# Performance work log

Hardware: AMD Instinct MI355X
Metric: run time of the kernel (lower is better)

## Reference

```python
import jax, jax.numpy as jnp
import numpy as np
from itertools import permutations

B, T, A, NIN = 10, 100, 20, 4096
NIMG, NATT, NPHYS = 1024, 512, 256


def _build_perm():
    # all 190 unordered pairs of 20 agents, lexicographically sorted (matches np.unique on sorted perms)
    perm = np.unique(np.sort(np.array(list(permutations(range(A), 2))), axis=1), axis=0)  # (190, 2)
    # for each agent k: the 19 pair-indices containing k, ordered (k in col0 first, then col1) as in torch code
    perm_ind = np.stack([
        np.hstack((np.where(perm[:, 0] == k)[0], np.where(perm[:, 1] == k)[0])) for k in range(A)
    ])  # (20, 19)
    return perm.astype(np.int32), perm_ind.astype(np.int32)

PERM, PERM_IND = _build_perm()


def setup_inputs() -> dict:
    key = jax.random.key(0)
    ks = jax.random.split(key, 7)
    def lin(k, out_f, in_f):
        return (jax.random.normal(k, (out_f, in_f), jnp.float32) / np.float32(np.sqrt(in_f)))
    return {
        "x": jax.random.normal(ks[0], (B, T, A, NIN), jnp.float32),
        "world_coord_feat": jax.random.normal(ks[1], (B, T, A, 13), jnp.float32),
        "W_glob": lin(ks[2], NIMG, NIN), "b_glob": jnp.zeros((NIMG,), jnp.float32),
        "W_loc": lin(ks[3], NATT, NIN), "b_loc": jnp.zeros((NATT,), jnp.float32),
        "W_phys": lin(ks[4], NPHYS, 26), "b_phys": jnp.zeros((NPHYS,), jnp.float32),
        "W_phys3": lin(ks[5], NPHYS, NPHYS), "b_phys3": jnp.zeros((NPHYS,), jnp.float32),
    }


def reference(x, world_coord_feat, W_glob, b_glob, W_loc, b_loc, W_phys, b_phys, W_phys3, b_phys3):
    pa = jnp.asarray(PERM)        # (190, 2)
    pind = jnp.asarray(PERM_IND)  # (20, 19)
    # global / local embeddings
    glob_embed = x[:, :, 0, :] @ W_glob.T + b_glob          # (B, T, NIMG)
    loc_embed = x[:, :, 1:, :] @ W_loc.T + b_loc            # (B, T, 19, NATT)
    # pairwise physical features: concat coords of both agents of each pair
    perm_feat = jnp.concatenate(
        [world_coord_feat[:, :, pa[:, 0], :], world_coord_feat[:, :, pa[:, 1], :]], axis=-1
    )                                                        # (B, T, 190, 26)
    # dropout layers are identity at inference; mask is computed but unused in original
    h1 = jax.nn.relu(perm_feat @ W_phys.T + b_phys)          # (B, T, 190, NPHYS)
    phys = h1 @ W_phys3.T + b_phys3                          # (B, T, 190, NPHYS)
    # per-agent gather of its 19 pairs + max-pool over pairs (fused segment-max)
    agent_tensor = jnp.max(phys[:, :, pind, :], axis=3)      # (B, T, 20, NPHYS)
    return glob_embed, loc_embed, agent_tensor
```

## Files before the change

### kernel.cpp

```cpp
#include <hip/hip_runtime.h>
#include <stdint.h>

typedef __bf16 bf16x8 __attribute__((ext_vector_type(8)));
typedef float  f32x4  __attribute__((ext_vector_type(4)));

__device__ __forceinline__ bf16x8 cvt8(const float* __restrict__ p) {
    float4 lo = *(const float4*)p;
    float4 hi = *(const float4*)(p + 4);
    bf16x8 r;
    r[0] = (__bf16)lo.x; r[1] = (__bf16)lo.y; r[2] = (__bf16)lo.z; r[3] = (__bf16)lo.w;
    r[4] = (__bf16)hi.x; r[5] = (__bf16)hi.y; r[6] = (__bf16)hi.z; r[7] = (__bf16)hi.w;
    return r;
}

__device__ __forceinline__ bf16x8 pack8(float4 lo, float4 hi) {
    bf16x8 r;
    r[0] = (__bf16)lo.x; r[1] = (__bf16)lo.y; r[2] = (__bf16)lo.z; r[3] = (__bf16)lo.w;
    r[4] = (__bf16)hi.x; r[5] = (__bf16)hi.y; r[6] = (__bf16)hi.z; r[7] = (__bf16)hi.w;
    return r;
}

__device__ __forceinline__ int pidx(int i, int j) {
    return i * 19 - (i * (i - 1)) / 2 + (j - i - 1);
}

template <int MODE, bool A_BF16, bool OUT_BF16>
__global__ __launch_bounds__(256) void gemm_bias_kernel(
    const void* __restrict__ Xv,
    const float* __restrict__ W,
    const float* __restrict__ bias,
    void* __restrict__ Cv,
    int M, int N, int K)
{
    __shared__ __bf16 As[64][40];
    __shared__ __bf16 Bs[64][40];

    const int tid  = threadIdx.x;
    const int srow = tid >> 2;
    const int scol = (tid & 3) << 3;

    int gmrow = (int)blockIdx.y * 64 + srow;
    int rA = gmrow < M ? gmrow : M - 1;
    size_t aoff;
    if (MODE == 0)      aoff = (size_t)rA * 81920;
    else if (MODE == 1) aoff = ((size_t)(rA / 19) * 20 + (size_t)(rA % 19) + 1) * 4096;
    else                aoff = (size_t)rA * (size_t)K;
    const float*  aptrF = (const float*)Xv  + aoff + scol;
    const __bf16* aptrH = (const __bf16*)Xv + aoff + scol;
    const float*  bptr  = W + (size_t)((int)blockIdx.x * 64 + srow) * (size_t)K + scol;

    const int w    = tid >> 6;
    const int lane = tid & 63;
    const int wm   = (w >> 1) * 32;
    const int wn   = (w & 1) * 32;
    const int l    = lane & 15;
    const int qk   = lane >> 4;
    const int q8   = qk * 8;

    f32x4 acc00 = {}, acc01 = {}, acc10 = {}, acc11 = {};

    for (int k0 = 0; k0 < K; k0 += 32) {
        bf16x8 av, bv;
        if (A_BF16) av = *(const bf16x8*)(aptrH + k0);
        else        av = cvt8(aptrF + k0);
        bv = cvt8(bptr + k0);
        __syncthreads();
        *(bf16x8*)&As[srow][scol] = av;
        *(bf16x8*)&Bs[srow][scol] = bv;
        __syncthreads();
        bf16x8 a0 = *(const bf16x8*)&As[wm + l][q8];
        bf16x8 a1 = *(const bf16x8*)&As[wm + 16 + l][q8];
        bf16x8 b0 = *(const bf16x8*)&Bs[wn + l][q8];
        bf16x8 b1 = *(const bf16x8*)&Bs[wn + 16 + l][q8];
        acc00 = __builtin_amdgcn_mfma_f32_16x16x32_bf16(a0, b0, acc00, 0, 0, 0);
        acc01 = __builtin_amdgcn_mfma_f32_16x16x32_bf16(a0, b1, acc01, 0, 0, 0);
        acc10 = __builtin_amdgcn_mfma_f32_16x16x32_bf16(a1, b0, acc10, 0, 0, 0);
        acc11 = __builtin_amdgcn_mfma_f32_16x16x32_bf16(a1, b1, acc11, 0, 0, 0);
    }

    const int colBase = (int)blockIdx.x * 64;
    const int rowBase = (int)blockIdx.y * 64;
    const float bias0 = bias[colBase + wn + l];
    const float bias1 = bias[colBase + wn + 16 + l];
    #pragma unroll
    for (int i = 0; i < 2; ++i) {
        f32x4 aj0 = (i == 0) ? acc00 : acc10;
        f32x4 aj1 = (i == 0) ? acc01 : acc11;
        #pragma unroll
        for (int r = 0; r < 4; ++r) {
            int row = rowBase + wm + i * 16 + qk * 4 + r;
            if (row < M) {
                size_t base = (size_t)row * (size_t)N + colBase + wn;
                float v0 = aj0[r] + bias0;
                float v1 = aj1[r] + bias1;
                if (OUT_BF16) {
                    ((__bf16*)Cv)[base + l]      = (__bf16)v0;
                    ((__bf16*)Cv)[base + 16 + l] = (__bf16)v1;
                } else {
                    ((float*)Cv)[base + l]      = v0;
                    ((float*)Cv)[base + 16 + l] = v1;
                }
            }
        }
    }
}

__global__ __launch_bounds__(256) void gemm_loc_v2(
    const float* __restrict__ X,
    const float* __restrict__ W,
    const float* __restrict__ bias,
    float* __restrict__ C)
{
    constexpr int M = 19000, N = 512, K = 4096;
    __shared__ __bf16 As[2][128][40];
    __shared__ __bf16 Bs[2][128][40];

    const int gx = 4, nwg = 596;
    int lid = (int)blockIdx.y * gx + (int)blockIdx.x;
    {
        int q = nwg >> 3, r = nwg & 7;
        int xcd = lid & 7, idx = lid >> 3;
        lid = (xcd < r ? xcd * (q + 1) : r * (q + 1) + (xcd - r) * q) + idx;
    }
    const int tx = lid % gx;
    const int ty = lid / gx;

    const int tid  = threadIdx.x;
    const int srow = tid >> 2;
    const int scol = (tid & 3) << 3;

    int gr0 = ty * 128 + srow;      int rA0 = gr0 < M ? gr0 : M - 1;
    int gr1 = gr0 + 64;             int rA1 = gr1 < M ? gr1 : M - 1;
    const float* aptr0 = X + ((size_t)(rA0 / 19) * 20 + (size_t)(rA0 % 19) + 1) * 4096 + scol;
    const float* aptr1 = X + ((size_t)(rA1 / 19) * 20 + (size_t)(rA1 % 19) + 1) * 4096 + scol;
    const float* bptr0 = W + (size_t)(tx * 128 + srow) * (size_t)K + scol;
    const float* bptr1 = W + (size_t)(tx * 128 + 64 + srow) * (size_t)K + scol;

    const int w    = tid >> 6;
    const int lane = tid & 63;
    const int wm   = (w >> 1) * 64;
    const int wn   = (w & 1) * 64;
    const int l    = lane & 15;
    const int qk   = lane >> 4;
    const int q8   = qk << 3;

    f32x4 acc[4][4];
    #pragma unroll
    for (int m = 0; m < 4; ++m)
        #pragma unroll
        for (int n = 0; n < 4; ++n) { f32x4 z = {0.f, 0.f, 0.f, 0.f}; acc[m][n] = z; }

    float4 sa0l, sa0h, sa1l, sa1h, sb0l, sb0h, sb1l, sb1h;

    sa0l = *(const float4*)(aptr0);     sa0h = *(const float4*)(aptr0 + 4);
    sa1l = *(const float4*)(aptr1);     sa1h = *(const float4*)(aptr1 + 4);
    sb0l = *(const float4*)(bptr0);     sb0h = *(const float4*)(bptr0 + 4);
    sb1l = *(const float4*)(bptr1);     sb1h = *(const float4*)(bptr1 + 4);
    *(bf16x8*)&As[0][srow][scol]      = pack8(sa0l, sa0h);
    *(bf16x8*)&As[0][srow + 64][scol] = pack8(sa1l, sa1h);
    *(bf16x8*)&Bs[0][srow][scol]      = pack8(sb0l, sb0h);
    *(bf16x8*)&Bs[0][srow + 64][scol] = pack8(sb1l, sb1h);

    int cur = 0;
    for (int i = 0; i < K / 32; ++i) {
        __syncthreads();
        if (i + 1 < K / 32) {
            int k0 = (i + 1) << 5;
            sa0l = *(const float4*)(aptr0 + k0); sa0h = *(const float4*)(aptr0 + k0 + 4);
            sa1l = *(const float4*)(aptr1 + k0); sa1h = *(const float4*)(aptr1 + k0 + 4);
            sb0l = *(const float4*)(bptr0 + k0); sb0h = *(const float4*)(bptr0 + k0 + 4);
            sb1l = *(const float4*)(bptr1 + k0); sb1h = *(const float4*)(bptr1 + k0 + 4);
        }
        bf16x8 af[4], bfr[4];
        #pragma unroll
        for (int m = 0; m < 4; ++m) af[m]  = *(const bf16x8*)&As[cur][wm + m * 16 + l][q8];
        #pragma unroll
        for (int n = 0; n < 4; ++n) bfr[n] = *(const bf16x8*)&Bs[cur][wn + n * 16 + l][q8];
        #pragma unroll
        for (int m = 0; m < 4; ++m)
            #pragma unroll
            for (int n = 0; n < 4; ++n)
                acc[m][n] = __builtin_amdgcn_mfma_f32_16x16x32_bf16(af[m], bfr[n], acc[m][n], 0, 0, 0);
        if (i + 1 < K / 32) {
            int nb = cur ^ 1;
            *(bf16x8*)&As[nb][srow][scol]      = pack8(sa0l, sa0h);
            *(bf16x8*)&As[nb][srow + 64][scol] = pack8(sa1l, sa1h);
            *(bf16x8*)&Bs[nb][srow][scol]      = pack8(sb0l, sb0h);
            *(bf16x8*)&Bs[nb][srow + 64][scol] = pack8(sb1l, sb1h);
        }
        cur ^= 1;
    }

    const int colBase = tx * 128 + wn;
    const int rowBase = ty * 128 + wm;
    float bs[4];
    #pragma unroll
    for (int n = 0; n < 4; ++n) bs[n] = bias[colBase + n * 16 + l];
    #pragma unroll
    for (int m = 0; m < 4; ++m) {
        #pragma unroll
        for (int r = 0; r < 4; ++r) {
            int row = rowBase + m * 16 + qk * 4 + r;
            if (row < M) {
                size_t base = (size_t)row * (size_t)N + colBase;
                #pragma unroll
                for (int n = 0; n < 4; ++n)
                    C[base + n * 16 + l] = acc[m][n][r] + bs[n];
            }
        }
    }
}

__global__ __launch_bounds__(256) void phys1_kernel(
    const float* __restrict__ wcf,
    const float* __restrict__ W1,
    const float* __restrict__ b1,
    __bf16* __restrict__ h1)
{
    __shared__ float fs[260];
    const int g = blockIdx.x;
    const int c = threadIdx.x;
    for (int i = c; i < 260; i += 256) fs[i] = wcf[g * 260 + i];
    float wrow[26];
    #pragma unroll
    for (int k = 0; k < 26; ++k) wrow[k] = W1[c * 26 + k];
    const float bias = b1[c];
    __syncthreads();

    __bf16* out = h1 + (size_t)g * 190 * 256 + c;
    int p = 0;
    for (int i = 0; i < 20; ++i) {
        for (int j = i + 1; j < 20; ++j, ++p) {
            float s = bias;
            #pragma unroll
            for (int k = 0; k < 13; ++k) s += wrow[k]      * fs[i * 13 + k];
            #pragma unroll
            for (int k = 0; k < 13; ++k) s += wrow[13 + k] * fs[j * 13 + k];
            out[(size_t)p * 256] = (__bf16)(s > 0.f ? s : 0.f);
        }
    }
}

__global__ __launch_bounds__(256) void segmax_kernel(
    const __bf16* __restrict__ phys,
    float* __restrict__ agent)
{
    const int a = blockIdx.x;
    const int g = blockIdx.y;
    const int c = threadIdx.x;
    const __bf16* base = phys + (size_t)g * 190 * 256 + c;
    float m = -3.4e38f;
    #pragma unroll
    for (int j = 0; j < 20; ++j) {
        if (j == a) continue;
        int p = (j > a) ? pidx(a, j) : pidx(j, a);
        float v = (float)base[(size_t)p * 256];
        m = v > m ? v : m;
    }
    agent[((size_t)g * 20 + a) * 256 + c] = m;
}

extern "C" void kernel_launch(void* const* d_in, const int* in_sizes, int n_in,
                              void* d_out, int out_size, void* d_ws, size_t ws_size,
                              hipStream_t stream)
{
    const float* x   = (const float*)d_in[0];
    const float* wcf = (const float*)d_in[1];
    const float* Wg  = (const float*)d_in[2];
    const float* bg  = (const float*)d_in[3];
    const float* Wl  = (const float*)d_in[4];
    const float* bl  = (const float*)d_in[5];
    const float* W1  = (const float*)d_in[6];
    const float* b1  = (const float*)d_in[7];
    const float* W3  = (const float*)d_in[8];
    const float* b3  = (const float*)d_in[9];

    float* out   = (float*)d_out;
    float* glob  = out;
    float* loc   = out + 1024000;
    float* agent = out + 1024000 + 9728000;

    __bf16* h1   = (__bf16*)d_ws;
    __bf16* phys = h1 + (size_t)190000 * 256;

    gemm_bias_kernel<0, false, false><<<dim3(1024 / 64, (1000 + 63) / 64), 256, 0, stream>>>(
        x, Wg, bg, glob, 1000, 1024, 4096);
    gemm_loc_v2<<<dim3(4, 149), 256, 0, stream>>>(x, Wl, bl, loc);
    phys1_kernel<<<1000, 256, 0, stream>>>(wcf, W1, b1, h1);
    gemm_bias_kernel<2, true, true><<<dim3(256 / 64, (190000 + 63) / 64), 256, 0, stream>>>(
        h1, W3, b3, phys, 190000, 256, 256);
    segmax_kernel<<<dim3(20, 1000), 256, 0, stream>>>(phys, agent);
}
```

Baseline: 903.6 us.

## Use 8-wave 128x128 tiles for loc GEMM and a dedicated phys2 GEMM

The loc GEMM moves from 4 waves to 8 waves per 128x128 tile. Each thread now stages one A row and one B row instead of two, and each wave covers a 64x32 sub-tile, which halves the per-wave accumulators and staging registers. The phys second-layer GEMM drops the generic 64x64 gemm_bias_kernel for a new specialised kernel of the same 8-wave 128x128 design, reading bf16 activations directly and writing bf16 output. The aim is more latency hiding and better tile reuse. The cost is more LDS fragment reads per MFMA and extra syncs shared across more waves.

```diff
diff --git a/kernel.cpp b/kernel.cpp
--- a/kernel.cpp
+++ b/kernel.cpp
@@ -105,7 +105,7 @@
     }
 }
 
-__global__ __launch_bounds__(256) void gemm_loc_v2(
+__global__ __launch_bounds__(512) void gemm_loc_w8(
     const float* __restrict__ X,
     const float* __restrict__ W,
     const float* __restrict__ bias,
@@ -129,73 +129,63 @@
     const int srow = tid >> 2;
     const int scol = (tid & 3) << 3;
 
-    int gr0 = ty * 128 + srow;      int rA0 = gr0 < M ? gr0 : M - 1;
-    int gr1 = gr0 + 64;             int rA1 = gr1 < M ? gr1 : M - 1;
-    const float* aptr0 = X + ((size_t)(rA0 / 19) * 20 + (size_t)(rA0 % 19) + 1) * 4096 + scol;
-    const float* aptr1 = X + ((size_t)(rA1 / 19) * 20 + (size_t)(rA1 % 19) + 1) * 4096 + scol;
-    const float* bptr0 = W + (size_t)(tx * 128 + srow) * (size_t)K + scol;
-    const float* bptr1 = W + (size_t)(tx * 128 + 64 + srow) * (size_t)K + scol;
+    int gr = ty * 128 + srow;
+    int rA = gr < M ? gr : M - 1;
+    const float* aptr = X + ((size_t)(rA / 19) * 20 + (size_t)(rA % 19) + 1) * 4096 + scol;
+    const float* bptr = W + (size_t)(tx * 128 + srow) * (size_t)K + scol;
 
     const int w    = tid >> 6;
     const int lane = tid & 63;
-    const int wm   = (w >> 1) * 64;
-    const int wn   = (w & 1) * 64;
+    const int wm   = (w >> 2) * 64;
+    const int wn   = (w & 3) * 32;
     const int l    = lane & 15;
     const int qk   = lane >> 4;
     const int q8   = qk << 3;
 
-    f32x4 acc[4][4];
+    f32x4 acc[4][2];
     #pragma unroll
     for (int m = 0; m < 4; ++m)
         #pragma unroll
-        for (int n = 0; n < 4; ++n) { f32x4 z = {0.f, 0.f, 0.f, 0.f}; acc[m][n] = z; }
-
-    float4 sa0l, sa0h, sa1l, sa1h, sb0l, sb0h, sb1l, sb1h;
-
-    sa0l = *(const float4*)(aptr0);     sa0h = *(const float4*)(aptr0 + 4);
-    sa1l = *(const float4*)(aptr1);     sa1h = *(const float4*)(aptr1 + 4);
-    sb0l = *(const float4*)(bptr0);     sb0h = *(const float4*)(bptr0 + 4);
-    sb1l = *(const float4*)(bptr1);     sb1h = *(const float4*)(bptr1 + 4);
-    *(bf16x8*)&As[0][srow][scol]      = pack8(sa0l, sa0h);
-    *(bf16x8*)&As[0][srow + 64][scol] = pack8(sa1l, sa1h);
-    *(bf16x8*)&Bs[0][srow][scol]      = pack8(sb0l, sb0h);
-    *(bf16x8*)&Bs[0][srow + 64][scol] = pack8(sb1l, sb1h);
+        for (int n = 0; n < 2; ++n) { f32x4 z = {0.f, 0.f, 0.f, 0.f}; acc[m][n] = z; }
+
+    float4 sal, sah, sbl, sbh;
+
+    sal = *(const float4*)(aptr);     sah = *(const float4*)(aptr + 4);
+    sbl = *(const float4*)(bptr);     sbh = *(const float4*)(bptr + 4);
+    *(bf16x8*)&As[0][srow][scol] = pack8(sal, sah);
+    *(bf16x8*)&Bs[0][srow][scol] = pack8(sbl, sbh);
 
     int cur = 0;
     for (int i = 0; i < K / 32; ++i) {
         __syncthreads();
         if (i + 1 < K / 32) {
             int k0 = (i + 1) << 5;
-            sa0l = *(const float4*)(aptr0 + k0); sa0h = *(const float4*)(aptr0 + k0 + 4);
-            sa1l = *(const float4*)(aptr1 + k0); sa1h = *(const float4*)(aptr1 + k0 + 4);
-            sb0l = *(const float4*)(bptr0 + k0); sb0h = *(const float4*)(bptr0 + k0 + 4);
-            sb1l = *(const float4*)(bptr1 + k0); sb1h = *(const float4*)(bptr1 + k0 + 4);
-        }
-        bf16x8 af[4], bfr[4];
+            sal = *(const float4*)(aptr + k0); sah = *(const float4*)(aptr + k0 + 4);
+            sbl = *(const float4*)(bptr + k0); sbh = *(const float4*)(bptr + k0 + 4);
+        }
+        bf16x8 af[4], bfr[2];
         #pragma unroll
         for (int m = 0; m < 4; ++m) af[m]  = *(const bf16x8*)&As[cur][wm + m * 16 + l][q8];
         #pragma unroll
-        for (int n = 0; n < 4; ++n) bfr[n] = *(const bf16x8*)&Bs[cur][wn + n * 16 + l][q8];
+        for (int n = 0; n < 2; ++n) bfr[n] = *(const bf16x8*)&Bs[cur][wn + n * 16 + l][q8];
         #pragma unroll
         for (int m = 0; m < 4; ++m)
             #pragma unroll
-            for (int n = 0; n < 4; ++n)
+            for (int n = 0; n < 2; ++n)
                 acc[m][n] = __builtin_amdgcn_mfma_f32_16x16x32_bf16(af[m], bfr[n], acc[m][n], 0, 0, 0);
         if (i + 1 < K / 32) {
             int nb = cur ^ 1;
-            *(bf16x8*)&As[nb][srow][scol]      = pack8(sa0l, sa0h);
-            *(bf16x8*)&As[nb][srow + 64][scol] = pack8(sa1l, sa1h);
-            *(bf16x8*)&Bs[nb][srow][scol]      = pack8(sb0l, sb0h);
-            *(bf16x8*)&Bs[nb][srow + 64][scol] = pack8(sb1l, sb1h);
+            *(bf16x8*)&As[nb][srow][scol] = pack8(sal, sah);
+            *(bf16x8*)&Bs[nb][srow][scol] = pack8(sbl, sbh);
         }
         cur ^= 1;
     }
 
     const int colBase = tx * 128 + wn;
     const int rowBase = ty * 128 + wm;
-    float bs[4];
-    #pragma unroll
-    for (int n = 0; n < 4; ++n) bs[n] = bias[colBase + n * 16 + l];
+    float bs[2];
+    #pragma unroll
+    for (int n = 0; n < 2; ++n) bs[n] = bias[colBase + n * 16 + l];
     #pragma unroll
     for (int m = 0; m < 4; ++m) {
         #pragma unroll
@@ -204,8 +194,105 @@
             if (row < M) {
                 size_t base = (size_t)row * (size_t)N + colBase;
                 #pragma unroll
-                for (int n = 0; n < 4; ++n)
+                for (int n = 0; n < 2; ++n)
                     C[base + n * 16 + l] = acc[m][n][r] + bs[n];
+            }
+        }
+    }
+}
+
+__global__ __launch_bounds__(512) void gemm_phys2_w8(
+    const __bf16* __restrict__ Xh,
+    const float* __restrict__ W,
+    const float* __restrict__ bias,
+    __bf16* __restrict__ C)
+{
+    constexpr int M = 190000, N = 256, K = 256;
+    __shared__ __bf16 As[2][128][40];
+    __shared__ __bf16 Bs[2][128][40];
+
+    const int gx = 2, nwg = 2970;
+    int lid = (int)blockIdx.y * gx + (int)blockIdx.x;
+    {
+        int q = nwg >> 3, r = nwg & 7;
+        int xcd = lid & 7, idx = lid >> 3;
+        lid = (xcd < r ? xcd * (q + 1) : r * (q + 1) + (xcd - r) * q) + idx;
+    }
+    const int tx = lid % gx;
+    const int ty = lid / gx;
+
+    const int tid  = threadIdx.x;
+    const int srow = tid >> 2;
+    const int scol = (tid & 3) << 3;
+
+    int gr = ty * 128 + srow;
+    int rA = gr < M ? gr : M - 1;
+    const __bf16* aptr = Xh + (size_t)rA * (size_t)K + scol;
+    const float*  bptr = W + (size_t)(tx * 128 + srow) * (size_t)K + scol;
+
+    const int w    = tid >> 6;
+    const int lane = tid & 63;
+    const int wm   = (w >> 2) * 64;
+    const int wn   = (w & 3) * 32;
+    const int l    = lane & 15;
+    const int qk   = lane >> 4;
+    const int q8   = qk << 3;
+
+    f32x4 acc[4][2];
+    #pragma unroll
+    for (int m = 0; m < 4; ++m)
+        #pragma unroll
+        for (int n = 0; n < 2; ++n) { f32x4 z = {0.f, 0.f, 0.f, 0.f}; acc[m][n] = z; }
+
+    bf16x8 sav;
+    float4 sbl, sbh;
+
+    sav = *(const bf16x8*)(aptr);
+    sbl = *(const float4*)(bptr);     sbh = *(const float4*)(bptr + 4);
+    *(bf16x8*)&As[0][srow][scol] = sav;
+    *(bf16x8*)&Bs[0][srow][scol] = pack8(sbl, sbh);
+
+    int cur = 0;
+    for (int i = 0; i < K / 32; ++i) {
+        __syncthreads();
+        if (i + 1 < K / 32) {
+            int k0 = (i + 1) << 5;
+            sav = *(const bf16x8*)(aptr + k0);
+            sbl = *(const float4*)(bptr + k0); sbh = *(const float4*)(bptr + k0 + 4);
+        }
+        bf16x8 af[4], bfr[2];
+        #pragma unroll
+        for (int m = 0; m < 4; ++m) af[m]  = *(const bf16x8*)&As[cur][wm + m * 16 + l][q8];
+        #pragma unroll
+        for (int n = 0; n < 2; ++n) bfr[n] = *(const bf16x8*)&Bs[cur][wn + n * 16 + l][q8];
+        #pragma unroll
+        for (int m = 0; m < 4; ++m)
+            #pragma unroll
+            for (int n = 0; n < 2; ++n)
+                acc[m][n] = __builtin_amdgcn_mfma_f32_16x16x32_bf16(af[m], bfr[n], acc[m][n], 0, 0, 0);
+        if (i + 1 < K / 32) {
+            int nb = cur ^ 1;
+            *(bf16x8*)&As[nb][srow][scol] = sav;
+            *(bf16x8*)&Bs[nb][srow][scol] = pack8(sbl, sbh);
+        }
+        cur ^= 1;
+    }
+
+    const int colBase = tx * 128 + wn;
+    const int rowBase = ty * 128 + wm;
+    float bs[2];
+    #pragma unroll
+    for (int n = 0; n < 2; ++n) bs[n] = bias[colBase + n * 16 + l];
+    #pragma unroll
+    for (int m = 0; m < 4; ++m) {
+        #pragma unroll
+        for (int r = 0; r < 4; ++r) {
+            int row = rowBase + m * 16 + qk * 4 + r;
+            if (row < M) {
+                size_t base = (size_t)row * (size_t)N + colBase;
+                #pragma unroll
+                for (int n = 0; n < 2; ++n)
+                    C[base + n * 16 + l] = (__bf16)(acc[m][n][r] + bs[n]);
             }
         }
     }
@@ -285,9 +372,8 @@
 
     gemm_bias_kernel<0, false, false><<<dim3(1024 / 64, (1000 + 63) / 64), 256, 0, stream>>>(
         x, Wg, bg, glob, 1000, 1024, 4096);
-    gemm_loc_v2<<<dim3(4, 149), 256, 0, stream>>>(x, Wl, bl, loc);
+    gemm_loc_w8<<<dim3(4, 149), 512, 0, stream>>>(x, Wl, bl, loc);
     phys1_kernel<<<1000, 256, 0, stream>>>(wcf, W1, b1, h1);
-    gemm_bias_kernel<2, true, true><<<dim3(256 / 64, (190000 + 63) / 64), 256, 0, stream>>>(
-        h1, W3, b3, phys, 190000, 256, 256);
+    gemm_phys2_w8<<<dim3(2, 1485), 512, 0, stream>>>(h1, W3, b3, phys);
     segmax_kernel<<<dim3(20, 1000), 256, 0, stream>>>(phys, agent);
 }
```

Result: no change. 899.0 us (-0.5%).
